# Performance work log

Hardware: AMD Instinct MI355X
Metric: run time of the kernel (lower is better)

## Reference

```python
import jax, jax.numpy as jnp
import numpy as np

N_PATCHES = 14
PS = 16            # patch size: 224 / 14
C, H_IMG, W_IMG = 3, 224, 224
HIDDEN = 768
HEADS = 12
DH = HIDDEN // HEADS
BLOCKS = 12
MLP = 4 * HIDDEN
OUT = 1000
SEQ = N_PATCHES ** 2 + 1  # 197
BATCH = 64


def get_positional_embeddings(seq_len, d):
    # sin(i/10000^(j/d)) for even j, cos(i/10000^((j-1)/d)) for odd j
    i = jnp.arange(seq_len, dtype=jnp.float32)[:, None]
    j = jnp.arange(d)[None, :]
    even = (j % 2 == 0)
    expo = jnp.where(even, j, j - 1).astype(jnp.float32) / d
    ang = i / (10000.0 ** expo)
    return jnp.where(even, jnp.sin(ang), jnp.cos(ang))


def layernorm(x, g, b, eps=1e-5):
    mu = x.mean(-1, keepdims=True)
    var = ((x - mu) ** 2).mean(-1, keepdims=True)
    return (x - mu) / jnp.sqrt(var + eps) * g + b


def mhsa(x, qw, qb, kw, kb, vw, vb):
    # x: [B,S,HIDDEN]; per-head linears qw/kw/vw: [H,DH,DH] (torch Linear weight layout)
    B, S, _ = x.shape
    xh = x.reshape(B, S, HEADS, DH)
    q = jnp.einsum('bshd,hed->bshe', xh, qw) + qb
    k = jnp.einsum('bshd,hed->bshe', xh, kw) + kb
    v = jnp.einsum('bshd,hed->bshe', xh, vw) + vb
    scores = jnp.einsum('bshe,bthe->bhst', q, k) / jnp.sqrt(jnp.float32(DH))
    attn = jax.nn.softmax(scores, axis=-1)
    out = jnp.einsum('bhst,bthe->bshe', attn, v)
    return out.reshape(B, S, HIDDEN)


def vit_block(x, p):
    ln1_g, ln1_b, qw, qb, kw, kb, vw, vb, ln2_g, ln2_b, w1, b1, w2, b2 = p
    x = x + mhsa(layernorm(x, ln1_g, ln1_b), qw, qb, kw, kb, vw, vb)
    h = layernorm(x, ln2_g, ln2_b)
    h = jax.nn.gelu(h @ w1.T + b1, approximate=False) @ w2.T + b2
    return x + h


def patchify(images):
    # [N,C,H,W] -> [N, n_patches^2, C*PS*PS], channel-major within each patch
    n = images.shape[0]
    x = images.reshape(n, C, N_PATCHES, PS, N_PATCHES, PS)
    x = x.transpose(0, 2, 4, 1, 3, 5)  # n, pi, pj, c, ps, ps
    return x.reshape(n, N_PATCHES * N_PATCHES, C * PS * PS)


def setup_inputs() -> dict:
    key = jax.random.key(0)
    ks = jax.random.split(key, 20)
    s = 0.02
    return {
        'images': jax.random.normal(ks[0], (BATCH, C, H_IMG, W_IMG), jnp.float32),
        'mapper_w': jax.random.normal(ks[1], (HIDDEN, C * PS * PS), jnp.float32) * s,
        'mapper_b': jnp.zeros((HIDDEN,), jnp.float32),
        'cls_token': jax.random.uniform(ks[2], (1, HIDDEN), jnp.float32),
        'ln1_g': jnp.ones((BLOCKS, HIDDEN), jnp.float32),
        'ln1_b': jnp.zeros((BLOCKS, HIDDEN), jnp.float32),
        'qw': jax.random.normal(ks[3], (BLOCKS, HEADS, DH, DH), jnp.float32) * s,
        'qb': jnp.zeros((BLOCKS, HEADS, DH), jnp.float32),
        'kw': jax.random.normal(ks[4], (BLOCKS, HEADS, DH, DH), jnp.float32) * s,
        'kb': jnp.zeros((BLOCKS, HEADS, DH), jnp.float32),
        'vw': jax.random.normal(ks[5], (BLOCKS, HEADS, DH, DH), jnp.float32) * s,
        'vb': jnp.zeros((BLOCKS, HEADS, DH), jnp.float32),
        'ln2_g': jnp.ones((BLOCKS, HIDDEN), jnp.float32),
        'ln2_b': jnp.zeros((BLOCKS, HIDDEN), jnp.float32),
        'w1': jax.random.normal(ks[6], (BLOCKS, MLP, HIDDEN), jnp.float32) * s,
        'b1': jnp.zeros((BLOCKS, MLP), jnp.float32),
        'w2': jax.random.normal(ks[7], (BLOCKS, HIDDEN, MLP), jnp.float32) * s,
        'b2': jnp.zeros((BLOCKS, HIDDEN), jnp.float32),
        'head_w': jax.random.normal(ks[8], (OUT, HIDDEN), jnp.float32) * s,
        'head_b': jnp.zeros((OUT,), jnp.float32),
    }


def reference(images, mapper_w, mapper_b, cls_token, ln1_g, ln1_b, qw, qb, kw, kb,
              vw, vb, ln2_g, ln2_b, w1, b1, w2, b2, head_w, head_b):
    n = images.shape[0]
    patches = patchify(images)
    tokens = patches @ mapper_w.T + mapper_b                      # [B, 196, HIDDEN]
    cls = jnp.broadcast_to(cls_token[None], (n, 1, HIDDEN))
    tokens = jnp.concatenate([cls, tokens], axis=1)               # [B, 197, HIDDEN]
    out = tokens + get_positional_embeddings(SEQ, HIDDEN)[None]

    stacked = (ln1_g, ln1_b, qw, qb, kw, kb, vw, vb, ln2_g, ln2_b, w1, b1, w2, b2)

    def step(x, p):
        return vit_block(x, p), None

    out, _ = jax.lax.scan(step, out, stacked)
    cls_out = out[:, 0]                                           # [B, HIDDEN]
    return jax.nn.softmax(cls_out @ head_w.T + head_b, axis=-1)
```

## Files before the change

### kernel.cpp

```cpp
#include <hip/hip_runtime.h>
#include <cstdint>
#include <cstddef>
#include <cstdio>

using u16 = unsigned short;
using u32 = unsigned int;

typedef __attribute__((ext_vector_type(8))) __bf16 bf16x8;
typedef __attribute__((ext_vector_type(4))) float f32x4;

struct alignas(16) U128 { u32 w[4]; };
struct alignas(16) F4   { float x[4]; };
struct alignas(8)  US4  { u16 h[4]; };

#define DEVFN static __device__ __forceinline__

DEVFN u16 f2bf(float x) {
  union { float f; u32 u; } v; v.f = x;
  u32 r = v.u + 0x7fffu + ((v.u >> 16) & 1u);
  return (u16)(r >> 16);
}

DEVFN bf16x8 ld16(const u16* p) { return __builtin_bit_cast(bf16x8, *(const U128*)p); }

DEVFN f32x4 mfma16(bf16x8 a, bf16x8 b, f32x4 c) {
  return __builtin_amdgcn_mfma_f32_16x16x32_bf16(a, b, c, 0, 0, 0);
}

DEVFN void gload_lds16(const u16* g, u16* l) {
  __builtin_amdgcn_global_load_lds(
      (const __attribute__((address_space(1))) void*)g,
      (__attribute__((address_space(3))) void*)l, 16, 0, 0);
}

DEVFN float gelu(float x) {
  float z = fabsf(x) * 0.70710678118f;
  float t = __builtin_amdgcn_rcpf(1.f + 0.3275911f * z);
  float p = t * (0.254829592f + t * (-0.284496736f + t * (1.421413741f +
            t * (-1.453152027f + t * 1.061405429f))));
  float e = __expf(-z * z);
  float erfz = 1.f - p * e;
  erfz = copysignf(erfz, x);
  return 0.5f * x * (1.f + erfz);
}

DEVFN void remap_bid(int bid, int Mb, int Nb, int& bm, int& bn) {
  const int ngrp  = Mb >> 3;
  const int per   = Nb << 3;
  const int nfull = ngrp * per;
  if (bid < nfull) {
    const int bmg = bid / per;
    const int rem = bid - bmg * per;
    bn = rem >> 3;
    bm = (bmg << 3) + (rem & 7);
  } else {
    const int r = bid - nfull;
    const int q = r / Nb;
    bm = (ngrp << 3) + q;
    bn = r - q * Nb;
  }
}

constexpr int SEQL   = 197;
constexpr int NB     = 64;
constexpr int NH     = 12;
constexpr int MROWS  = NB * SEQL;
constexpr int MPAD   = 12672;
constexpr int MPATCH = NB * 196;
constexpr int SP     = 208;
constexpr int SP2    = 224;
constexpr int BHN    = NB * NH;

constexpr size_t OFF_X    = 0;
constexpr size_t OFF_ALN  = OFF_X    + (size_t)MPAD * 768 * 4;
constexpr size_t OFF_H    = OFF_ALN  + (size_t)MPAD * 768 * 2;
constexpr size_t OFF_WQKV = OFF_H    + (size_t)MPAD * 3072 * 2;
constexpr size_t OFF_W1   = OFF_WQKV + (size_t)2304 * 128 * 2;
constexpr size_t OFF_W2   = OFF_W1   + (size_t)3072 * 768 * 2;
constexpr size_t OFF_WMAP = OFF_W2   + (size_t)3072 * 768 * 2;
constexpr size_t OFF_Q    = OFF_WMAP + (size_t)768 * 768 * 2;
constexpr size_t OFF_K    = OFF_Q    + (size_t)BHN * SP * 64 * 2;
constexpr size_t OFF_VT   = OFF_K    + (size_t)BHN * SP * 64 * 2;
constexpr size_t OFF_PAT  = OFF_VT   + (size_t)BHN * 64 * SP2 * 2;
constexpr size_t OFF_POS  = OFF_PAT  + (size_t)MPATCH * 768 * 2;
constexpr size_t WS_NEED  = OFF_POS  + (size_t)SEQL * 768 * 4;

__global__ void zero_kernel(u32* __restrict__ p, long n) {
  long i = (long)blockIdx.x * 256 + threadIdx.x;
  long stride = (long)gridDim.x * 256;
  for (; i < n; i += stride) p[i] = 0u;
}

__global__ void cvt_kernel(const float* __restrict__ src, u16* __restrict__ dst, int n) {
  int i = blockIdx.x * 256 + threadIdx.x;
  if (i < n) dst[i] = f2bf(src[i]);
}

__global__ void pos_kernel(float* __restrict__ pos) {
  int i = blockIdx.x * 256 + threadIdx.x;
  if (i >= SEQL * 768) return;
  int s = i / 768, j = i - s * 768;
  float expo = (float)(j & ~1) * (1.0f / 768.0f);
  float ang  = (float)s * expf(-expo * logf(10000.0f));
  pos[i] = (j & 1) ? cosf(ang) : sinf(ang);
}

__global__ void cls_kernel(const float* __restrict__ cls, const float* __restrict__ pos,
                           float* __restrict__ X) {
  int b = blockIdx.x;
  for (int c = threadIdx.x; c < 768; c += 256)
    X[(size_t)b * SEQL * 768 + c] = cls[c] + pos[c];
}

__global__ void patchify_kernel(const float* __restrict__ img, u16* __restrict__ out) {
  int i = blockIdx.x * 256 + threadIdx.x;
  if (i >= MPATCH * 768) return;
  int m = i / 768, k = i - m * 768;
  int b = m / 196, p = m - b * 196;
  int py = p / 14, px = p - py * 14;
  int c = k >> 8, rem = k & 255, iy = rem >> 4, ix = rem & 15;
  float v = img[(((size_t)b * 3 + c) * 224 + py * 16 + iy) * 224 + px * 16 + ix];
  out[i] = f2bf(v);
}

__global__ void build_wqkv2(const float* __restrict__ qw, const float* __restrict__ kw,
                            const float* __restrict__ vw, u16* __restrict__ W, int blk) {
  int i = blockIdx.x * 256 + threadIdx.x;
  if (i >= 2304 * 128) return;
  int n = i >> 7, kk = i & 127;
  int p = n / 768, ef = n - p * 768;
  int h = ef >> 6, e = ef & 63;
  float v = 0.f;
  if ((kk >> 6) == (h & 1)) {
    int d = kk & 63;
    const float* w = (p == 0) ? qw : (p == 1) ? kw : vw;
    v = w[(((size_t)blk * NH + h) * 64 + e) * 64 + d];
  }
  W[i] = f2bf(v);
}

__global__ __launch_bounds__(256) void ln_kernel(const float* __restrict__ X,
    const float* __restrict__ g, const float* __restrict__ b, u16* __restrict__ out) {
  int row  = blockIdx.x * 4 + (threadIdx.x >> 6);
  int lane = threadIdx.x & 63;
  const float* x = X + (size_t)row * 768 + lane * 12;
  F4 a0 = *(const F4*)(x);
  F4 a1 = *(const F4*)(x + 4);
  F4 a2 = *(const F4*)(x + 8);
  float v[12];
  #pragma unroll
  for (int j = 0; j < 4; ++j) { v[j] = a0.x[j]; v[4 + j] = a1.x[j]; v[8 + j] = a2.x[j]; }
  float s = 0.f, q = 0.f;
  #pragma unroll
  for (int j = 0; j < 12; ++j) { s += v[j]; q += v[j] * v[j]; }
  #pragma unroll
  for (int d = 1; d < 64; d <<= 1) { s += __shfl_xor(s, d); q += __shfl_xor(q, d); }
  float mu  = s * (1.f / 768.f);
  float var = q * (1.f / 768.f) - mu * mu;
  float rs  = rsqrtf(var + 1e-5f);
  const float* gp = g + lane * 12;
  const float* bp = b + lane * 12;
  u16* op = out + (size_t)row * 768 + lane * 12;
  u16 o[12];
  #pragma unroll
  for (int j = 0; j < 12; ++j) o[j] = f2bf((v[j] - mu) * rs * gp[j] + bp[j]);
  #pragma unroll
  for (int c = 0; c < 3; ++c) {
    US4 w; w.h[0] = o[c*4]; w.h[1] = o[c*4+1]; w.h[2] = o[c*4+2]; w.h[3] = o[c*4+3];
    *(US4*)(op + c * 4) = w;
  }
}

enum { EPI_PATCH = 0, EPI_QKV = 1, EPI_GELU = 2, EPI_RESID = 3 };

template<int EPI>
__global__ __launch_bounds__(256, 2) void gemm3s(
    const u16* __restrict__ A, const u16* __restrict__ B, int K, int Mb, int Nb,
    const float* __restrict__ e0, float* __restrict__ f0, u16* __restrict__ o0) {
  __shared__ u16 Ab[3][128 * 32];
  __shared__ u16 Bb[3][256 * 32];
  const int wave = threadIdx.x >> 6, lane = threadIdx.x & 63;
  const int fr = lane & 15, fg = lane >> 4;
  int bm, bn;
  remap_bid(blockIdx.x, Mb, Nb, bm, bn);
  const int srow = wave * 16 + (lane >> 2);
  const int gcol = ((lane & 3) ^ ((lane >> 3) & 3)) * 8;
  const u16* gA = A + (size_t)(bm * 128 + srow) * K + gcol;
  const u16* gB = B + (size_t)(bn * 256 + srow) * K + gcol;
  const int nt = K >> 5;
  const int sl = (fg ^ ((fr >> 1) & 3)) * 8;

  auto STAGE = [&](int c, int t) {
    #pragma unroll
    for (int s = 0; s < 2; ++s)
      gload_lds16(gA + t * 32 + (size_t)(s * 64) * K, &Ab[c][0] + wave * 512 + s * 2048);
    #pragma unroll
    for (int s = 0; s < 4; ++s)
      gload_lds16(gB + t * 32 + (size_t)(s * 64) * K, &Bb[c][0] + wave * 512 + s * 2048);
  };

  f32x4 acc[8][4] = {};

  auto COMPUTE = [&](int c) {
    const u16* ab = &Ab[c][0];
    const u16* bb = &Bb[c][0];
    bf16x8 af[8], bf[4];
    #pragma unroll
    for (int i = 0; i < 8; ++i) af[i] = ld16(ab + (i * 16 + fr) * 32 + sl);
    #pragma unroll
    for (int j = 0; j < 4; ++j) bf[j] = ld16(bb + (wave * 64 + j * 16 + fr) * 32 + sl);
    __builtin_amdgcn_s_setprio(1);
    #pragma unroll
    for (int i = 0; i < 8; ++i)
      #pragma unroll
      for (int j = 0; j < 4; ++j)
        acc[i][j] = mfma16(af[i], bf[j], acc[i][j]);
    __builtin_amdgcn_s_setprio(0);
  };

  STAGE(0, 0);
  STAGE(1, 1);
  int cur = 0;
  for (int t = 0; t + 2 < nt; ++t) {
    int nxt = cur + 2; if (nxt >= 3) nxt -= 3;
    STAGE(nxt, t + 2);
    asm volatile("s_waitcnt vmcnt(12)" ::: "memory");
    __builtin_amdgcn_s_barrier();
    COMPUTE(cur);
    __builtin_amdgcn_s_barrier();
    cur = (cur + 1 == 3) ? 0 : cur + 1;
  }
  asm volatile("s_waitcnt vmcnt(6)" ::: "memory");
  __builtin_amdgcn_s_barrier();
  COMPUTE(cur);
  __builtin_amdgcn_s_barrier();
  cur = (cur + 1 == 3) ? 0 : cur + 1;
  asm volatile("s_waitcnt vmcnt(0)" ::: "memory");
  __builtin_amdgcn_s_barrier();
  COMPUTE(cur);

  #pragma unroll
  for (int i = 0; i < 8; ++i) {
    #pragma unroll
    for (int r = 0; r < 4; ++r) {
      const int m = bm * 128 + i * 16 + fg * 4 + r;
      if constexpr (EPI == EPI_GELU) {
        u16* hrow = o0 + (size_t)m * 3072;
        #pragma unroll
        for (int j = 0; j < 4; ++j) {
          const int n = bn * 256 + wave * 64 + j * 16 + fr;
          hrow[n] = f2bf(gelu(acc[i][j][r] + e0[n]));
        }
      } else {
        if (m < MROWS) {
          float* xrow = f0 + (size_t)m * 768;
          #pragma unroll
          for (int j = 0; j < 4; ++j) {
            const int n = bn * 256 + wave * 64 + j * 16 + fr;
            xrow[n] += acc[i][j][r] + e0[n];
          }
        }
      }
    }
  }
}

template<int EPI>
__global__ __launch_bounds__(256) void gemm_bt(
    const u16* __restrict__ A, const u16* __restrict__ B, int K, int lda, int ldb,
    int Mb, int Nb,
    const float* __restrict__ e0, const float* __restrict__ e1, const float* __restrict__ e2,
    float* __restrict__ f0, const float* __restrict__ f1,
    u16* __restrict__ o0, u16* __restrict__ o1, u16* __restrict__ o2) {
  __shared__ u16 Ab[2][128 * 32];
  __shared__ u16 Bb[2][128 * 32];
  const int tid  = threadIdx.x;
  const int wave = tid >> 6, lane = tid & 63;
  int bm, bn;
  remap_bid(blockIdx.x, Mb, Nb, bm, bn);
  const int fr = lane & 15, fg = lane >> 4;
  if constexpr (EPI == EPI_QKV) A += (bn % 6) * 128;
  const int srow = wave * 16 + (lane >> 2);
  const int gcol = ((lane & 3) ^ ((lane >> 3) & 3)) * 8;
  const u16* gA = A + (size_t)(bm * 128 + srow) * lda + gcol;
  const u16* gB = B + (size_t)(bn * 128 + srow) * ldb + gcol;
  const int wm = (wave >> 1) * 64, wn = (wave & 1) * 64;
  const int sx = (fr >> 1) & 3;
  const int nt = K >> 5;

  auto STAGE = [&](int b, int t) {
    #pragma unroll
    for (int s = 0; s < 2; ++s) {
      gload_lds16(gA + t * 32 + (size_t)s * 64 * lda, &Ab[b][0] + wave * 512 + s * 2048);
      gload_lds16(gB + t * 32 + (size_t)s * 64 * ldb, &Bb[b][0] + wave * 512 + s * 2048);
    }
  };

  f32x4 acc[4][4] = {};
  STAGE(0, 0);
  for (int t = 0; t < nt; ++t) {
    if (t + 1 < nt) {
      STAGE((t + 1) & 1, t + 1);
      asm volatile("s_waitcnt vmcnt(4)" ::: "memory");
    } else {
      asm volatile("s_waitcnt vmcnt(0)" ::: "memory");
    }
    __builtin_amdgcn_s_barrier();
    const u16* ab = &Ab[t & 1][0];
    const u16* bbuf = &Bb[t & 1][0];
    const int sl = (fg ^ sx) * 8;
    bf16x8 af[4], bfv[4];
    #pragma unroll
    for (int i = 0; i < 4; ++i) af[i]  = ld16(ab + (wm + i * 16 + fr) * 32 + sl);
    #pragma unroll
    for (int j = 0; j < 4; ++j) bfv[j] = ld16(bbuf + (wn + j * 16 + fr) * 32 + sl);
    __builtin_amdgcn_s_setprio(1);
    #pragma unroll
    for (int i = 0; i < 4; ++i)
      #pragma unroll
      for (int j = 0; j < 4; ++j)
        acc[i][j] = mfma16(af[i], bfv[j], acc[i][j]);
    __builtin_amdgcn_s_setprio(0);
    __builtin_amdgcn_s_barrier();
  }
  #pragma unroll
  for (int i = 0; i < 4; ++i) {
    #pragma unroll
    for (int r = 0; r < 4; ++r) {
      const int m = bm * 128 + wm + i * 16 + fg * 4 + r;
      if constexpr (EPI == EPI_PATCH) {
        const int bb = m / 196;
        const int s  = m - bb * 196 + 1;
        float* xrow = f0 + ((size_t)bb * SEQL + s) * 768;
        const float* prow = f1 + (size_t)s * 768;
        #pragma unroll
        for (int j = 0; j < 4; ++j) {
          const int n = bn * 128 + wn + j * 16 + fr;
          xrow[n] = acc[i][j][r] + e0[n] + prow[n];
        }
      } else if constexpr (EPI == EPI_QKV) {
        if (m < MROWS) {
          const int bb = m / 197;
          const int s  = m - bb * 197;
          #pragma unroll
          for (int j = 0; j < 4; ++j) {
            const int n = bn * 128 + wn + j * 16 + fr;
            const int p = n / 768;
            const int ef = n - p * 768;
            const int h = ef >> 6, e = ef & 63;
            const size_t bh = (size_t)bb * NH + h;
            if (p == 0)      o0[(bh * SP + s) * 64 + e] = f2bf((acc[i][j][r] + e0[ef]) * 0.125f);
            else if (p == 1) o1[(bh * SP + s) * 64 + e] = f2bf(acc[i][j][r] + e1[ef]);
            else             o2[(bh * 64 + e) * SP2 + s] = f2bf(acc[i][j][r] + e2[ef]);
          }
        }
      }
    }
  }
}

__global__ __launch_bounds__(256) void attn_kernel(const u16* __restrict__ Q,
    const u16* __restrict__ Km, const u16* __restrict__ Vt, float* __restrict__ X) {
  __shared__ u16  P[4][16 * SP2];
  __shared__ float sums[4][16];
  const int bh = blockIdx.x;
  const int b = bh / NH, h = bh - b * NH;
  const int wave = threadIdx.x >> 6, lane = threadIdx.x & 63;
  const int fr = lane & 15, fg = lane >> 4;
  const u16* Qb = Q  + (size_t)bh * SP * 64;
  const u16* Kb = Km + (size_t)bh * SP * 64;
  const u16* Vb = Vt + (size_t)bh * 64 * SP2;
  u16* Pl = &P[wave][0];
  for (int qt = wave; qt < 13; qt += 4) {
    const int s0 = qt * 16;
    bf16x8 qf0 = ld16(Qb + (size_t)(s0 + fr) * 64 + fg * 8);
    bf16x8 qf1 = ld16(Qb + (size_t)(s0 + fr) * 64 + 32 + fg * 8);
    f32x4 sc[13];
    #pragma unroll
    for (int tf = 0; tf < 13; ++tf) {
      f32x4 a = {0.f, 0.f, 0.f, 0.f};
      bf16x8 k0 = ld16(Kb + (size_t)(tf * 16 + fr) * 64 + fg * 8);
      bf16x8 k1 = ld16(Kb + (size_t)(tf * 16 + fr) * 64 + 32 + fg * 8);
      a = mfma16(qf0, k0, a);
      a = mfma16(qf1, k1, a);
      sc[tf] = a;
    }
    float mx[4] = {-3e38f, -3e38f, -3e38f, -3e38f};
    #pragma unroll
    for (int tf = 0; tf < 13; ++tf) {
      const bool ok = (tf * 16 + fr) < 197;
      #pragma unroll
      for (int r = 0; r < 4; ++r) {
        float v = ok ? sc[tf][r] : -3e38f;
        sc[tf][r] = v;
        mx[r] = fmaxf(mx[r], v);
      }
    }
    #pragma unroll
    for (int r = 0; r < 4; ++r)
      #pragma unroll
      for (int d = 1; d < 16; d <<= 1) mx[r] = fmaxf(mx[r], __shfl_xor(mx[r], d));
    float sm[4] = {0.f, 0.f, 0.f, 0.f};
    #pragma unroll
    for (int tf = 0; tf < 13; ++tf) {
      #pragma unroll
      for (int r = 0; r < 4; ++r) {
        float e = __expf(sc[tf][r] - mx[r]);
        sm[r] += e;
        Pl[(fg * 4 + r) * SP2 + tf * 16 + fr] = f2bf(e);
      }
    }
    #pragma unroll
    for (int r = 0; r < 4; ++r) {
      #pragma unroll
      for (int d = 1; d < 16; d <<= 1) sm[r] += __shfl_xor(sm[r], d);
      if (fr == 0) sums[wave][fg * 4 + r] = sm[r];
    }
    #pragma unroll
    for (int r = 0; r < 4; ++r) Pl[(fg * 4 + r) * SP2 + 208 + fr] = 0;
    f32x4 o[4] = {};
    #pragma unroll
    for (int ks = 0; ks < 7; ++ks) {
      bf16x8 pf = ld16(Pl + fr * SP2 + ks * 32 + fg * 8);
      #pragma unroll
      for (int ef = 0; ef < 4; ++ef) {
        bf16x8 vf = ld16(Vb + (size_t)(ef * 16 + fr) * SP2 + ks * 32 + fg * 8);
        o[ef] = mfma16(vf, pf, o[ef]);
      }
    }
    const float inv = 1.f / sums[wave][fr];
    const int s = s0 + fr;
    if (s < 197) {
      float* xp = X + ((size_t)b * SEQL + s) * 768 + h * 64;
      #pragma unroll
      for (int ef = 0; ef < 4; ++ef)
        #pragma unroll
        for (int r = 0; r < 4; ++r)
          xp[ef * 16 + fg * 4 + r] += o[ef][r] * inv;
    }
  }
}

__global__ __launch_bounds__(256) void head_kernel(const float* __restrict__ X,
    const float* __restrict__ hw, const float* __restrict__ hb, float* __restrict__ out) {
  __shared__ float xr[768];
  __shared__ float lg[1000];
  __shared__ float red[8];
  const int b = blockIdx.x, tid = threadIdx.x;
  for (int c = tid; c < 768; c += 256) xr[c] = X[(size_t)b * SEQL * 768 + c];
  __syncthreads();
  for (int n = tid; n < 1000; n += 256) {
    const F4* w4 = (const F4*)(hw + (size_t)n * 768);
    const F4* x4 = (const F4*)xr;
    float acc = hb[n];
    for (int k = 0; k < 192; ++k) {
      F4 w = w4[k]; F4 xv = x4[k];
      acc += w.x[0] * xv.x[0] + w.x[1] * xv.x[1] + w.x[2] * xv.x[2] + w.x[3] * xv.x[3];
    }
    lg[n] = acc;
  }
  __syncthreads();
  float m = -3e38f;
  for (int n = tid; n < 1000; n += 256) m = fmaxf(m, lg[n]);
  #pragma unroll
  for (int d = 1; d < 64; d <<= 1) m = fmaxf(m, __shfl_xor(m, d));
  if ((tid & 63) == 0) red[tid >> 6] = m;
  __syncthreads();
  m = fmaxf(fmaxf(red[0], red[1]), fmaxf(red[2], red[3]));
  float s = 0.f;
  for (int n = tid; n < 1000; n += 256) s += expf(lg[n] - m);
  #pragma unroll
  for (int d = 1; d < 64; d <<= 1) s += __shfl_xor(s, d);
  if ((tid & 63) == 0) red[4 + (tid >> 6)] = s;
  __syncthreads();
  s = red[4] + red[5] + red[6] + red[7];
  const float inv = 1.f / s;
  for (int n = tid; n < 1000; n += 256) out[(size_t)b * 1000 + n] = expf(lg[n] - m) * inv;
}

extern "C" void kernel_launch(void* const* d_in, const int* in_sizes, int n_in,
                              void* d_out, int out_size, void* d_ws, size_t ws_size,
                              hipStream_t stream) {
  (void)in_sizes; (void)n_in; (void)out_size;
  if (ws_size < WS_NEED) { printf("ws too small: %zu < %zu\n", ws_size, WS_NEED); return; }

  const float* images   = (const float*)d_in[0];
  const float* mapper_w = (const float*)d_in[1];
  const float* mapper_b = (const float*)d_in[2];
  const float* cls_tok  = (const float*)d_in[3];
  const float* ln1_g    = (const float*)d_in[4];
  const float* ln1_b    = (const float*)d_in[5];
  const float* qw       = (const float*)d_in[6];
  const float* qb       = (const float*)d_in[7];
  const float* kw       = (const float*)d_in[8];
  const float* kb       = (const float*)d_in[9];
  const float* vw       = (const float*)d_in[10];
  const float* vb       = (const float*)d_in[11];
  const float* ln2_g    = (const float*)d_in[12];
  const float* ln2_b    = (const float*)d_in[13];
  const float* w1       = (const float*)d_in[14];
  const float* b1       = (const float*)d_in[15];
  const float* w2       = (const float*)d_in[16];
  const float* b2       = (const float*)d_in[17];
  const float* head_w   = (const float*)d_in[18];
  const float* head_b   = (const float*)d_in[19];

  char* ws = (char*)d_ws;
  float* X    = (float*)(ws + OFF_X);
  u16*  Aln   = (u16*)(ws + OFF_ALN);
  u16*  Hb    = (u16*)(ws + OFF_H);
  u16*  Wqkv  = (u16*)(ws + OFF_WQKV);
  u16*  W1b   = (u16*)(ws + OFF_W1);
  u16*  W2b   = (u16*)(ws + OFF_W2);
  u16*  Wmap  = (u16*)(ws + OFF_WMAP);
  u16*  Qb    = (u16*)(ws + OFF_Q);
  u16*  Kb    = (u16*)(ws + OFF_K);
  u16*  Vtb   = (u16*)(ws + OFF_VT);
  u16*  Pat   = (u16*)(ws + OFF_PAT);
  float* Pos  = (float*)(ws + OFF_POS);

  zero_kernel<<<2048, 256, 0, stream>>>((u32*)Qb,  (long)(BHN * SP * 64 / 2));
  zero_kernel<<<2048, 256, 0, stream>>>((u32*)Kb,  (long)(BHN * SP * 64 / 2));
  zero_kernel<<<2048, 256, 0, stream>>>((u32*)Vtb, (long)(BHN * 64 * SP2 / 2));
  zero_kernel<<<64,   256, 0, stream>>>((u32*)(X + (size_t)MROWS * 768), (long)((MPAD - MROWS) * 768));

  pos_kernel<<<(SEQL * 768 + 255) / 256, 256, 0, stream>>>(Pos);
  cvt_kernel<<<(768 * 768 + 255) / 256, 256, 0, stream>>>(mapper_w, Wmap, 768 * 768);
  patchify_kernel<<<(MPATCH * 768 + 255) / 256, 256, 0, stream>>>(images, Pat);
  cls_kernel<<<NB, 256, 0, stream>>>(cls_tok, Pos, X);

  gemm_bt<EPI_PATCH><<<(MPATCH / 128) * (768 / 128), 256, 0, stream>>>(
      Pat, Wmap, 768, 768, 768, MPATCH / 128, 768 / 128,
      mapper_b, nullptr, nullptr, X, Pos, nullptr, nullptr, nullptr);

  for (int blk = 0; blk < 12; ++blk) {
    ln_kernel<<<MPAD / 4, 256, 0, stream>>>(X, ln1_g + blk * 768, ln1_b + blk * 768, Aln);
    build_wqkv2<<<(2304 * 128 + 255) / 256, 256, 0, stream>>>(qw, kw, vw, Wqkv, blk);
    gemm_bt<EPI_QKV><<<(MPAD / 128) * (2304 / 128), 256, 0, stream>>>(
        Aln, Wqkv, 128, 768, 128, MPAD / 128, 2304 / 128,
        qb + blk * 768, kb + blk * 768, vb + blk * 768,
        nullptr, nullptr, Qb, Kb, Vtb);
    attn_kernel<<<BHN, 256, 0, stream>>>(Qb, Kb, Vtb, X);
    ln_kernel<<<MPAD / 4, 256, 0, stream>>>(X, ln2_g + blk * 768, ln2_b + blk * 768, Aln);
    cvt_kernel<<<(3072 * 768 + 255) / 256, 256, 0, stream>>>(w1 + (size_t)blk * 3072 * 768, W1b, 3072 * 768);
    gemm3s<EPI_GELU><<<(MPAD / 128) * (3072 / 256), 256, 0, stream>>>(
        Aln, W1b, 768, MPAD / 128, 3072 / 256, b1 + blk * 3072, nullptr, Hb);
    cvt_kernel<<<(3072 * 768 + 255) / 256, 256, 0, stream>>>(w2 + (size_t)blk * 768 * 3072, W2b, 768 * 3072);
    gemm3s<EPI_RESID><<<(MPAD / 128) * (768 / 256), 256, 0, stream>>>(
        Hb, W2b, 3072, MPAD / 128, 768 / 256, b2 + blk * 768, X, nullptr);
  }

  head_kernel<<<NB, 256, 0, stream>>>(X, head_w, head_b, (float*)d_out);
}
```

Measured before the change: 4.586 ms.

## Replace MLP GEMM with 256x256 tile, 8-wave, K=64 double-buffered kernel

The two MLP GEMMs move from a 128x256 tile, 4-wave, triple-buffered K=32 kernel to a 256x256 tile with 8 waves (2x4), K-step 64, and a double buffer. The next stage's global-to-LDS loads are interleaved between MFMA sub-blocks. The larger tile is meant to raise reuse per LDS byte and cut barrier and loop overhead. To fit the 256-row tile, M is padded to 12800, which means extra zeroed rows and more wasted compute on the padding. The larger LDS footprint (128KB) also limits occupancy.

After: 4.329 ms. 1.06x faster.

```diff
diff --git a/kernel.cpp b/kernel.cpp
--- a/kernel.cpp
+++ b/kernel.cpp
@@ -66,6 +66,7 @@
 constexpr int NH     = 12;
 constexpr int MROWS  = NB * SEQL;
 constexpr int MPAD   = 12672;
+constexpr int MPAD2  = 12800;
 constexpr int MPATCH = NB * 196;
 constexpr int SP     = 208;
 constexpr int SP2    = 224;
@@ -73,8 +74,8 @@
 
 constexpr size_t OFF_X    = 0;
 constexpr size_t OFF_ALN  = OFF_X    + (size_t)MPAD * 768 * 4;
-constexpr size_t OFF_H    = OFF_ALN  + (size_t)MPAD * 768 * 2;
-constexpr size_t OFF_WQKV = OFF_H    + (size_t)MPAD * 3072 * 2;
+constexpr size_t OFF_H    = OFF_ALN  + (size_t)MPAD2 * 768 * 2;
+constexpr size_t OFF_WQKV = OFF_H    + (size_t)MPAD2 * 3072 * 2;
 constexpr size_t OFF_W1   = OFF_WQKV + (size_t)2304 * 128 * 2;
 constexpr size_t OFF_W2   = OFF_W1   + (size_t)3072 * 768 * 2;
 constexpr size_t OFF_WMAP = OFF_W2   + (size_t)3072 * 768 * 2;
@@ -174,81 +175,123 @@
 enum { EPI_PATCH = 0, EPI_QKV = 1, EPI_GELU = 2, EPI_RESID = 3 };
 
 template<int EPI>
-__global__ __launch_bounds__(256, 2) void gemm3s(
+__global__ __launch_bounds__(512, 2) void gemm8p(
     const u16* __restrict__ A, const u16* __restrict__ B, int K, int Mb, int Nb,
     const float* __restrict__ e0, float* __restrict__ f0, u16* __restrict__ o0) {
-  __shared__ u16 Ab[3][128 * 32];
-  __shared__ u16 Bb[3][256 * 32];
-  const int wave = threadIdx.x >> 6, lane = threadIdx.x & 63;
+  __shared__ u16 Ab[2][256 * 64];
+  __shared__ u16 Bb[2][256 * 64];
+  const int tid = threadIdx.x;
+  const int wave = tid >> 6, lane = tid & 63;
   const int fr = lane & 15, fg = lane >> 4;
+  const int wm2 = wave >> 2, wn4 = wave & 3;
   int bm, bn;
   remap_bid(blockIdx.x, Mb, Nb, bm, bn);
-  const int srow = wave * 16 + (lane >> 2);
-  const int gcol = ((lane & 3) ^ ((lane >> 3) & 3)) * 8;
-  const u16* gA = A + (size_t)(bm * 128 + srow) * K + gcol;
-  const u16* gB = B + (size_t)(bn * 256 + srow) * K + gcol;
-  const int nt = K >> 5;
-  const int sl = (fg ^ ((fr >> 1) & 3)) * 8;
-
-  auto STAGE = [&](int c, int t) {
-    #pragma unroll
-    for (int s = 0; s < 2; ++s)
-      gload_lds16(gA + t * 32 + (size_t)(s * 64) * K, &Ab[c][0] + wave * 512 + s * 2048);
-    #pragma unroll
-    for (int s = 0; s < 4; ++s)
-      gload_lds16(gB + t * 32 + (size_t)(s * 64) * K, &Bb[c][0] + wave * 512 + s * 2048);
+
+  const int sr   = tid >> 3;
+  const int scol = (((tid & 7) ^ (sr & 7)) * 8);
+  const u16* gAb = A + (size_t)(bm * 256 + sr) * K + scol;
+  const u16* gBb = B + (size_t)(bn * 256 + sr) * K + scol;
+
+  const int ns = K >> 6;
+
+  auto STAGE_A = [&](int b, int t) {
+    u16* d = &Ab[b][0] + wave * 512;
+    const u16* g = gAb + (size_t)t * 64;
+    gload_lds16(g,                   d);
+    gload_lds16(g + (size_t)64 * K,  d + 4096);
+    gload_lds16(g + (size_t)128 * K, d + 8192);
+    gload_lds16(g + (size_t)192 * K, d + 12288);
   };
+  auto STAGE_B = [&](int b, int t) {
+    u16* d = &Bb[b][0] + wave * 512;
+    const u16* g = gBb + (size_t)t * 64;
+    gload_lds16(g,                   d);
+    gload_lds16(g + (size_t)64 * K,  d + 4096);
+    gload_lds16(g + (size_t)128 * K, d + 8192);
+    gload_lds16(g + (size_t)192 * K, d + 12288);
+  };
+
+  const int rdA = (wm2 * 128 + fr) * 64;
+  const int rdB = (wn4 * 64 + fr) * 64;
+  const int slx = fr & 7;
+  const int sl0 = ((fg) ^ slx) * 8;
+  const int sl1 = ((4 + fg) ^ slx) * 8;
 
   f32x4 acc[8][4] = {};
 
-  auto COMPUTE = [&](int c) {
-    const u16* ab = &Ab[c][0];
-    const u16* bb = &Bb[c][0];
-    bf16x8 af[8], bf[4];
-    #pragma unroll
-    for (int i = 0; i < 8; ++i) af[i] = ld16(ab + (i * 16 + fr) * 32 + sl);
-    #pragma unroll
-    for (int j = 0; j < 4; ++j) bf[j] = ld16(bb + (wave * 64 + j * 16 + fr) * 32 + sl);
-    __builtin_amdgcn_s_setprio(1);
-    #pragma unroll
-    for (int i = 0; i < 8; ++i)
-      #pragma unroll
-      for (int j = 0; j < 4; ++j)
-        acc[i][j] = mfma16(af[i], bf[j], acc[i][j]);
-    __builtin_amdgcn_s_setprio(0);
-  };
-
-  STAGE(0, 0);
-  STAGE(1, 1);
-  int cur = 0;
-  for (int t = 0; t + 2 < nt; ++t) {
-    int nxt = cur + 2; if (nxt >= 3) nxt -= 3;
-    STAGE(nxt, t + 2);
-    asm volatile("s_waitcnt vmcnt(12)" ::: "memory");
-    __builtin_amdgcn_s_barrier();
-    COMPUTE(cur);
-    __builtin_amdgcn_s_barrier();
-    cur = (cur + 1 == 3) ? 0 : cur + 1;
-  }
-  asm volatile("s_waitcnt vmcnt(6)" ::: "memory");
-  __builtin_amdgcn_s_barrier();
-  COMPUTE(cur);
-  __builtin_amdgcn_s_barrier();
-  cur = (cur + 1 == 3) ? 0 : cur + 1;
+  STAGE_A(0, 0);
+  STAGE_B(0, 0);
   asm volatile("s_waitcnt vmcnt(0)" ::: "memory");
   __builtin_amdgcn_s_barrier();
-  COMPUTE(cur);
+
+  for (int s = 0; s < ns; ++s) {
+    const int b = s & 1;
+    const bool pf = (s + 1 < ns);
+    const u16* ab = &Ab[b][0];
+    const u16* bbuf = &Bb[b][0];
+    bf16x8 af[4], bfv[4];
+
+    #pragma unroll
+    for (int a = 0; a < 4; ++a) af[a] = ld16(ab + rdA + a * 1024 + sl0);
+    #pragma unroll
+    for (int j = 0; j < 4; ++j) bfv[j] = ld16(bbuf + rdB + j * 1024 + sl0);
+    if (pf) STAGE_A(b ^ 1, s + 1);
+    __builtin_amdgcn_s_setprio(1);
+    #pragma unroll
+    for (int a = 0; a < 4; ++a)
+      #pragma unroll
+      for (int j = 0; j < 4; ++j)
+        acc[a][j] = mfma16(af[a], bfv[j], acc[a][j]);
+    __builtin_amdgcn_s_setprio(0);
+
+    #pragma unroll
+    for (int a = 0; a < 4; ++a) af[a] = ld16(ab + rdA + 4096 + a * 1024 + sl0);
+    if (pf) STAGE_B(b ^ 1, s + 1);
+    __builtin_amdgcn_s_setprio(1);
+    #pragma unroll
+    for (int a = 0; a < 4; ++a)
+      #pragma unroll
+      for (int j = 0; j < 4; ++j)
+        acc[4 + a][j] = mfma16(af[a], bfv[j], acc[4 + a][j]);
+    __builtin_amdgcn_s_setprio(0);
+
+    #pragma unroll
+    for (int a = 0; a < 4; ++a) af[a] = ld16(ab + rdA + a * 1024 + sl1);
+    #pragma unroll
+    for (int j = 0; j < 4; ++j) bfv[j] = ld16(bbuf + rdB + j * 1024 + sl1);
+    __builtin_amdgcn_s_setprio(1);
+    #pragma unroll
+    for (int a = 0; a < 4; ++a)
+      #pragma unroll
+      for (int j = 0; j < 4; ++j)
+        acc[a][j] = mfma16(af[a], bfv[j], acc[a][j]);
+    __builtin_amdgcn_s_setprio(0);
+
+    #pragma unroll
+    for (int a = 0; a < 4; ++a) af[a] = ld16(ab + rdA + 4096 + a * 1024 + sl1);
+    __builtin_amdgcn_s_setprio(1);
+    #pragma unroll
+    for (int a = 0; a < 4; ++a)
+      #pragma unroll
+      for (int j = 0; j < 4; ++j)
+        acc[4 + a][j] = mfma16(af[a], bfv[j], acc[4 + a][j]);
+    __builtin_amdgcn_s_setprio(0);
+
+    asm volatile("s_waitcnt vmcnt(0)" ::: "memory");
+    __builtin_amdgcn_s_barrier();
+  }
 
   #pragma unroll
   for (int i = 0; i < 8; ++i) {
+    const int ro = (i >> 2) * 64 + (i & 3) * 16;
     #pragma unroll
     for (int r = 0; r < 4; ++r) {
-      const int m = bm * 128 + i * 16 + fg * 4 + r;
+      const int m = bm * 256 + wm2 * 128 + ro + fg * 4 + r;
       if constexpr (EPI == EPI_GELU) {
         u16* hrow = o0 + (size_t)m * 3072;
         #pragma unroll
         for (int j = 0; j < 4; ++j) {
-          const int n = bn * 256 + wave * 64 + j * 16 + fr;
+          const int n = bn * 256 + wn4 * 64 + j * 16 + fr;
           hrow[n] = f2bf(gelu(acc[i][j][r] + e0[n]));
         }
       } else {
@@ -256,7 +299,7 @@
           float* xrow = f0 + (size_t)m * 768;
           #pragma unroll
           for (int j = 0; j < 4; ++j) {
-            const int n = bn * 256 + wave * 64 + j * 16 + fr;
+            const int n = bn * 256 + wn4 * 64 + j * 16 + fr;
             xrow[n] += acc[i][j][r] + e0[n];
           }
         }
@@ -523,6 +566,7 @@
   zero_kernel<<<2048, 256, 0, stream>>>((u32*)Kb,  (long)(BHN * SP * 64 / 2));
   zero_kernel<<<2048, 256, 0, stream>>>((u32*)Vtb, (long)(BHN * 64 * SP2 / 2));
   zero_kernel<<<64,   256, 0, stream>>>((u32*)(X + (size_t)MROWS * 768), (long)((MPAD - MROWS) * 768));
+  zero_kernel<<<48,   256, 0, stream>>>((u32*)(Aln + (size_t)MPAD * 768), (long)((MPAD2 - MPAD) * 768 / 2));
 
   pos_kernel<<<(SEQL * 768 + 255) / 256, 256, 0, stream>>>(Pos);
   cvt_kernel<<<(768 * 768 + 255) / 256, 256, 0, stream>>>(mapper_w, Wmap, 768 * 768);
@@ -543,11 +587,11 @@
     attn_kernel<<<BHN, 256, 0, stream>>>(Qb, Kb, Vtb, X);
     ln_kernel<<<MPAD / 4, 256, 0, stream>>>(X, ln2_g + blk * 768, ln2_b + blk * 768, Aln);
     cvt_kernel<<<(3072 * 768 + 255) / 256, 256, 0, stream>>>(w1 + (size_t)blk * 3072 * 768, W1b, 3072 * 768);
-    gemm3s<EPI_GELU><<<(MPAD / 128) * (3072 / 256), 256, 0, stream>>>(
-        Aln, W1b, 768, MPAD / 128, 3072 / 256, b1 + blk * 3072, nullptr, Hb);
+    gemm8p<EPI_GELU><<<(MPAD2 / 256) * (3072 / 256), 512, 0, stream>>>(
+        Aln, W1b, 768, MPAD2 / 256, 3072 / 256, b1 + blk * 3072, nullptr, Hb);
     cvt_kernel<<<(3072 * 768 + 255) / 256, 256, 0, stream>>>(w2 + (size_t)blk * 768 * 3072, W2b, 768 * 3072);
-    gemm3s<EPI_RESID><<<(MPAD / 128) * (768 / 256), 256, 0, stream>>>(
-        Hb, W2b, 3072, MPAD / 128, 768 / 256, b2 + blk * 768, X, nullptr);
+    gemm8p<EPI_RESID><<<(MPAD2 / 256) * (768 / 256), 512, 0, stream>>>(
+        Hb, W2b, 3072, MPAD2 / 256, 768 / 256, b2 + blk * 768, X, nullptr);
   }
 
   head_kernel<<<NB, 256, 0, stream>>>(X, head_w, head_b, (float*)d_out);
```
